# Kernel optimization log

Hardware: AMD Instinct MI355X
Metric: run time of the kernel (lower is better)

The kernel has to match this reference:

```python
import jax, jax.numpy as jnp
import numpy as np
from jax import lax

B, T, U, V, D, H = 4, 256, 64, 1024, 256, 256
BLANK = V - 1
NEG = -1.0e30
CTC_W = 0.3


def setup_inputs():
    ks = jax.random.split(jax.random.key(0), 9)
    return {
        "x_enc": jax.random.normal(ks[0], (B, T, D), jnp.float32),
        "x_dec": jax.random.normal(ks[1], (B, U + 1, H), jnp.float32),
        "W_enc": jax.random.normal(ks[2], (D, H), jnp.float32) / float(np.sqrt(D)),
        "b_enc": jnp.zeros((H,), jnp.float32),
        "W_dec": jax.random.normal(ks[3], (H, H), jnp.float32) / float(np.sqrt(H)),
        "b_dec": jnp.zeros((H,), jnp.float32),
        "W_out": jax.random.normal(ks[4], (H, V), jnp.float32) / float(np.sqrt(H)),
        "b_out": jnp.zeros((V,), jnp.float32),
        "W_ctc": jax.random.normal(ks[5], (D, V), jnp.float32) / float(np.sqrt(D)),
        "b_ctc": jnp.zeros((V,), jnp.float32),
        "target": jax.random.randint(ks[6], (B, U), 0, V - 1, jnp.int32),
        "frame_length": (T - jax.random.randint(ks[7], (B,), 0, T // 4)).astype(jnp.int32),
        "target_length": (U - jax.random.randint(ks[8], (B,), 0, U // 4)).astype(jnp.int32),
    }


def _forward(x_enc, x_dec, W_enc, b_enc, W_dec, b_dec, W_out, b_out, W_ctc, b_ctc,
             target, frame_length, target_length):
    b_idx = jnp.arange(B)
    ft, tl = frame_length, target_length

    # ---- Joiner: broadcast-add of projected enc/pred states, tanh, output proj ----
    h = jnp.tanh((x_enc @ W_enc + b_enc)[:, :, None, :]
                 + (x_dec @ W_dec + b_dec)[:, None, :, :])        # [B,T,U+1,H]
    logp = jax.nn.log_softmax(h @ W_out + b_out, axis=-1)          # [B,T,U+1,V]

    # gather=True trick: only blank and target-label log-probs are needed
    lp_blank = logp[..., BLANK]                                    # [B,T,U+1]
    lp_label = jnp.take_along_axis(
        logp[:, :, :U, :],
        jnp.broadcast_to(target[:, None, :, None], (B, T, U, 1)), axis=3)[..., 0]  # [B,T,U]

    # ---- RNNT forward DP over the (T, U+1) lattice ----
    def u_scan(b0, lbl):
        # b0[u] = alpha[t-1,u] + blank[t-1,u]; alpha[t,u] = logaddexp(b0[u], alpha[t,u-1]+lbl[u-1])
        def step(c, xs):
            bu, lu = xs
            new = jnp.logaddexp(bu, c + lu)
            return new, new
        _, outs = lax.scan(step, b0[:, 0],
                           (jnp.moveaxis(b0[:, 1:], 1, 0), jnp.moveaxis(lbl, 1, 0)))
        return jnp.concatenate([b0[:, :1], jnp.moveaxis(outs, 0, 1)], axis=1)

    alpha0 = jnp.concatenate([jnp.zeros((B, 1), logp.dtype),
                              jnp.cumsum(lp_label[:, 0, :], axis=1)], axis=1)  # [B,U+1]

    def t_step(prev, xs):
        blk_prev, lbl_t = xs
        a = u_scan(prev + blk_prev, lbl_t)
        return a, a

    _, rest = lax.scan(t_step, alpha0,
                       (jnp.moveaxis(lp_blank[:, :-1, :], 1, 0),
                        jnp.moveaxis(lp_label[:, 1:, :], 1, 0)))
    alphas = jnp.concatenate([alpha0[None], rest], axis=0)          # [T,B,U+1]
    ll = alphas[ft - 1, b_idx, tl] + lp_blank[b_idx, ft - 1, tl]
    rnnt_loss = jnp.mean(-ll)

    # ---- CTC branch: linear head on encoder output + standard CTC DP ----
    logp_ctc = jax.nn.log_softmax(x_enc @ W_ctc + b_ctc, axis=-1)   # [B,T,V]
    S = 2 * U + 1
    ext = jnp.full((B, S), BLANK, jnp.int32).at[:, 1::2].set(target)
    emit = jnp.take_along_axis(logp_ctc,
                               jnp.broadcast_to(ext[:, None, :], (B, T, S)), axis=2)  # [B,T,S]
    skip = jnp.concatenate([jnp.zeros((B, 2), bool),
                            (ext[:, 2:] != BLANK) & (ext[:, 2:] != ext[:, :-2])], axis=1)
    c0 = jnp.full((B, S), NEG, logp_ctc.dtype).at[:, 0].set(emit[:, 0, 0]).at[:, 1].set(emit[:, 0, 1])

    def c_step(prev, xs):
        emit_t, t = xs
        p2 = jnp.concatenate([jnp.full((B, 1), NEG, prev.dtype), prev[:, :-1]], axis=1)
        p3 = jnp.where(skip,
                       jnp.concatenate([jnp.full((B, 2), NEG, prev.dtype), prev[:, :-2]], axis=1),
                       NEG)
        new = emit_t + jnp.logaddexp(jnp.logaddexp(prev, p2), p3)
        new = jnp.where((t < ft)[:, None], new, prev)  # freeze past frame_length
        return new, None

    cT, _ = lax.scan(c_step, c0, (jnp.moveaxis(emit[:, 1:, :], 1, 0), jnp.arange(1, T)))
    s_last = 2 * tl
    ll_ctc = jnp.logaddexp(cT[b_idx, s_last], cT[b_idx, s_last - 1])
    ctc_loss = jnp.where(ll_ctc < NEG / 2, 0.0, -ll_ctc).sum() / B  # zero_infinity, sum/B

    return rnnt_loss + CTC_W * ctc_loss


def reference(x_enc, x_dec, W_enc, b_enc, W_dec, b_dec, W_out, b_out, W_ctc, b_ctc,
              target, frame_length, target_length):
    return _forward(x_enc, x_dec, W_enc, b_enc, W_dec, b_dec, W_out, b_out, W_ctc, b_ctc,
                    target, frame_length, target_length)
```

## Files before the change

### kernel.cpp

```cpp
#include <hip/hip_runtime.h>
#include <hip/hip_bf16.h>

#define Bn 4
#define Tn 256
#define Un 64
#define UP1 65
#define Vn 1024
#define Dn 256
#define Hn 256
#define BLANKC 1023
#define NEGF (-1.0e30f)
#define CTCW 0.3f
#define R2E 1.4426950408889634f
#define LN2 0.6931471805599453f

typedef __attribute__((ext_vector_type(8))) short short8;
typedef __attribute__((ext_vector_type(4))) float f32x4;
typedef __attribute__((ext_vector_type(4))) unsigned int u32x4;

static __device__ __forceinline__ unsigned short f2bf(float f) {
  unsigned int u = __float_as_uint(f);
  u += 0x7FFFu + ((u >> 16) & 1u);
  return (unsigned short)(u >> 16);
}
static __device__ __forceinline__ unsigned int pack2bf(float a, float b) {
  return (unsigned int)f2bf(a) | ((unsigned int)f2bf(b) << 16);
}
static __device__ __forceinline__ float ftanh(float x) {
  float e = __expf(2.0f * x);
  return 1.0f - 2.0f / (e + 1.0f);
}
static __device__ __forceinline__ float ex2(float x) {
  return __builtin_amdgcn_exp2f(x);
}
static __device__ __forceinline__ float lg2(float x) {
  return __builtin_amdgcn_logf(x);
}
static __device__ __forceinline__ float laddexp2_(float x, float y) {
  float m = fmaxf(x, y);
  float d = y - x;
  return m + lg2(1.0f + ex2(-fabsf(d)));
}
static __device__ __forceinline__ float laddexp3_2(float a, float b, float c) {
  float m = fmaxf(fmaxf(a, b), c);
  return m + lg2(ex2(a - m) + ex2(b - m) + ex2(c - m));
}
static __device__ __forceinline__ float shfl_up1(float x) {
  int r = __builtin_amdgcn_update_dpp(0, __float_as_int(x), 0x138, 0xF, 0xF, false);
  return __int_as_float(r);
}

__global__ __launch_bounds__(256) void k_prep(
    const float* __restrict__ W_enc, const float* __restrict__ W_dec,
    const float* __restrict__ W_out, const float* __restrict__ W_ctc,
    unsigned short* __restrict__ Wt_enc, unsigned short* __restrict__ Wt_dec,
    unsigned short* __restrict__ Wt_out, unsigned short* __restrict__ Wt_ctc,
    float* __restrict__ out) {
  const int blk = blockIdx.x, tid = threadIdx.x;
  if (blk == 0 && tid == 0) out[0] = 0.0f;
  __shared__ float tilebuf[64][65];
  if (blk < 128) {
    const float* Wsrc = (blk < 64) ? W_out : W_ctc;
    unsigned short* Wd = (blk < 64) ? Wt_out : Wt_ctc;
    const int tt = blk & 63;
    const int k0 = (tt & 3) * 64, v0 = (tt >> 2) * 64;
#pragma unroll
    for (int rep = 0; rep < 16; ++rep) {
      int e = rep * 256 + tid;
      int rr = e >> 6, cc = e & 63;
      tilebuf[rr][cc] = Wsrc[(k0 + rr) * 1024 + (v0 + cc)];
    }
    __syncthreads();
#pragma unroll
    for (int rep = 0; rep < 16; ++rep) {
      int e = rep * 256 + tid;
      int nn = e >> 6, kk = e & 63;
      int n = v0 + nn, k = k0 + kk;
      int c = n >> 8, col = n & 255;
      int ks = k >> 5, sub = (k >> 3) & 3, k7 = k & 7;
      Wd[(c * 8 + ks) * 8192 + sub * 2048 + col * 8 + k7] = f2bf(tilebuf[kk][nn]);
    }
  } else {
    const float* Wsrc = (blk < 144) ? W_enc : W_dec;
    unsigned short* Wd = (blk < 144) ? Wt_enc : Wt_dec;
    const int tt = (blk - 128) & 15;
    const int k0 = (tt & 3) * 64, v0 = (tt >> 2) * 64;
#pragma unroll
    for (int rep = 0; rep < 16; ++rep) {
      int e = rep * 256 + tid;
      int rr = e >> 6, cc = e & 63;
      tilebuf[rr][cc] = Wsrc[(k0 + rr) * 256 + (v0 + cc)];
    }
    __syncthreads();
#pragma unroll
    for (int rep = 0; rep < 16; ++rep) {
      int e = rep * 256 + tid;
      int rr = e >> 6, cc = e & 63;
      Wd[(v0 + rr) * 256 + (k0 + cc)] = f2bf(tilebuf[cc][rr]);
    }
  }
}

__global__ __launch_bounds__(256) void k_lin(
    const float* __restrict__ x_enc, const float* __restrict__ x_dec,
    const unsigned short* __restrict__ Wt_enc, const float* __restrict__ b_enc,
    const unsigned short* __restrict__ Wt_dec, const float* __restrict__ b_dec,
    float* __restrict__ enc_lin, float* __restrict__ dec_lin) {
  __shared__ __align__(16) char Asw[64 * 512];
  const int tid = threadIdx.x;
  const int w = tid >> 6, l = tid & 63;
  const int l15 = l & 15, l4 = l >> 4;
  const bool enc = blockIdx.x < 16;
  const int m0 = enc ? blockIdx.x * 64 : (blockIdx.x - 16) * 64;
  const int Mlim = enc ? 1024 : 260;
  const float* xp = enc ? x_enc : x_dec;
  const unsigned short* Wt = enc ? Wt_enc : Wt_dec;
  const float* bias = enc ? b_enc : b_dec;
  float* outp = enc ? enc_lin : dec_lin;

#pragma unroll
  for (int it = 0; it < 8; ++it) {
    int e = (it << 8) + tid;
    int i = e >> 5;
    int k0 = (e & 31) << 3;
    int r = m0 + i;
    if (r > Mlim - 1) r = Mlim - 1;
    const float* sp = xp + r * 256 + k0;
    f32x4 e0 = *(const f32x4*)sp;
    f32x4 e1 = *(const f32x4*)(sp + 4);
    u32x4 pv;
    pv[0] = pack2bf(e0[0], e0[1]);
    pv[1] = pack2bf(e0[2], e0[3]);
    pv[2] = pack2bf(e1[0], e1[1]);
    pv[3] = pack2bf(e1[2], e1[3]);
    int byt = (i << 9) + (k0 << 1);
    byt ^= (i & 7) << 4;
    *(u32x4*)(Asw + byt) = pv;
  }
  __syncthreads();

  const int nb = w * 64;
  f32x4 acc[4][4] = {};
#pragma unroll
  for (int ks = 0; ks < 8; ++ks) {
    int k = ks * 32 + l4 * 8;
    short8 af[4];
#pragma unroll
    for (int mt = 0; mt < 4; ++mt) {
      int i = mt * 16 + l15;
      int byt = (i << 9) + (k << 1);
      byt ^= (i & 7) << 4;
      af[mt] = *(const short8*)(Asw + byt);
    }
    short8 bfr[4];
#pragma unroll
    for (int nt = 0; nt < 4; ++nt) {
      int n = nb + nt * 16 + l15;
      bfr[nt] = *(const short8*)(Wt + n * 256 + k);
    }
#pragma unroll
    for (int mt = 0; mt < 4; ++mt)
#pragma unroll
      for (int nt = 0; nt < 4; ++nt)
        acc[mt][nt] = __builtin_amdgcn_mfma_f32_16x16x32_bf16(
            af[mt], bfr[nt], acc[mt][nt], 0, 0, 0);
  }
  float biasv[4];
#pragma unroll
  for (int nt = 0; nt < 4; ++nt) biasv[nt] = bias[nb + nt * 16 + l15];
#pragma unroll
  for (int mt = 0; mt < 4; ++mt)
#pragma unroll
    for (int rr = 0; rr < 4; ++rr) {
      int row = m0 + mt * 16 + l4 * 4 + rr;
      if (row < Mlim) {
#pragma unroll
        for (int nt = 0; nt < 4; ++nt)
          outp[row * 256 + nb + nt * 16 + l15] = acc[mt][nt][rr] + biasv[nt];
      }
    }
}

__global__ __launch_bounds__(512) void k_join2(
    const float* __restrict__ enc_lin, const float* __restrict__ dec_lin,
    const unsigned short* __restrict__ Wt_out, const float* __restrict__ b_out,
    const float* __restrict__ x_enc,
    const unsigned short* __restrict__ Wt_ctc, const float* __restrict__ b_ctc,
    const int* __restrict__ target,
    float* __restrict__ lp_blank, float* __restrict__ lp_label,
    float* __restrict__ ctc_blank, float* __restrict__ ctc_lse,
    float* __restrict__ ctc_lab) {
  __shared__ __align__(16) char Asw[128 * 512];
  __shared__ float s_psum[4][128];
  __shared__ float s_blank[128], s_label[128];
  __shared__ int s_tgt[128];

  const int tid = threadIdx.x;
  const int w = tid >> 6, l = tid & 63;
  const int wc = w & 3, wr = w >> 2;
  const int l15 = l & 15, l4 = l >> 4;
  const int bid = blockIdx.x;

  const bool joiner = bid >= 8;
  const unsigned short* Wt = joiner ? Wt_out : Wt_ctc;
  const float* bias = joiner ? b_out : b_ctc;

  const unsigned short* tb = Wt + l4 * 2048 + (wc * 64 + l15) * 8;

  short8 bE[4], bO[4];
#define LOADB(REG, S)                                                          \
  {                                                                            \
    const unsigned short* p_ = tb + (S)*8192;                                  \
    _Pragma("unroll") for (int nt = 0; nt < 4; ++nt)                           \
        REG[nt] = *(const short8*)(p_ + nt * 128);                             \
  }
  {
    const int sc0 = (bid & 3) * 8;
    LOADB(bE, sc0 + 0)
    LOADB(bO, sc0 + 1)
  }

  int b, r0 = 0, g0 = 0;
  if (joiner) {
    const int jbid = bid - 8;
    b = jbid / 130;
    r0 = (jbid % 130) * 128;
#pragma unroll
    for (int it = 0; it < 8; ++it) {
      int e = (it << 9) + tid;
      int i = e >> 5;
      int k0 = (e & 31) << 3;
      int r = r0 + i;
      int t = r / 65;
      int u = r - t * 65;
      const float* ep = enc_lin + ((b * Tn + t) * Hn + k0);
      const float* dp = dec_lin + ((b * UP1 + u) * Hn + k0);
      f32x4 e0 = *(const f32x4*)ep;
      f32x4 e1 = *(const f32x4*)(ep + 4);
      f32x4 d0 = *(const f32x4*)dp;
      f32x4 d1 = *(const f32x4*)(dp + 4);
      u32x4 pv;
      pv[0] = pack2bf(ftanh(e0[0] + d0[0]) * R2E, ftanh(e0[1] + d0[1]) * R2E);
      pv[1] = pack2bf(ftanh(e0[2] + d0[2]) * R2E, ftanh(e0[3] + d0[3]) * R2E);
      pv[2] = pack2bf(ftanh(e1[0] + d1[0]) * R2E, ftanh(e1[1] + d1[1]) * R2E);
      pv[3] = pack2bf(ftanh(e1[2] + d1[2]) * R2E, ftanh(e1[3] + d1[3]) * R2E);
      int byt = (i << 9) + (k0 << 1);
      byt ^= (i & 7) << 4;
      *(u32x4*)(Asw + byt) = pv;
    }
    if (tid < 128) {
      int u = (r0 + tid) % 65;
      s_tgt[tid] = (u < Un) ? target[b * Un + u] : -1;
    }
  } else {
    g0 = bid * 128;
    b = g0 >> 8;
#pragma unroll
    for (int it = 0; it < 8; ++it) {
      int e = (it << 9) + tid;
      int i = e >> 5;
      int k0 = (e & 31) << 3;
      const float* sp = x_enc + (g0 + i) * Dn + k0;
      f32x4 e0 = *(const f32x4*)sp;
      f32x4 e1 = *(const f32x4*)(sp + 4);
      u32x4 pv;
      pv[0] = pack2bf(e0[0] * R2E, e0[1] * R2E);
      pv[1] = pack2bf(e0[2] * R2E, e0[3] * R2E);
      pv[2] = pack2bf(e1[0] * R2E, e1[1] * R2E);
      pv[3] = pack2bf(e1[2] * R2E, e1[3] * R2E);
      int byt = (i << 9) + (k0 << 1);
      byt ^= (i & 7) << 4;
      *(u32x4*)(Asw + byt) = pv;
    }
    if (tid < 64) s_tgt[tid] = target[b * Un + tid];
  }
  __syncthreads();

  float ssum[16];
#pragma unroll
  for (int j = 0; j < 16; ++j) ssum[j] = 0.0f;

#define MFMASTEP(REG, KS)                                                      \
  {                                                                            \
    const int k_ = (KS)*32 + l4 * 8;                                           \
    _Pragma("unroll") for (int mt = 0; mt < 4; ++mt) {                         \
      int i_ = wr * 64 + mt * 16 + l15;                                        \
      int byt_ = ((i_ << 9) + (k_ << 1)) ^ ((i_ & 7) << 4);                    \
      short8 af_ = *(const short8*)(Asw + byt_);                               \
      _Pragma("unroll") for (int nt = 0; nt < 4; ++nt)                         \
          acc[mt][nt] = __builtin_amdgcn_mfma_f32_16x16x32_bf16(               \
              af_, REG[nt], acc[mt][nt], 0, 0, 0);                             \
    }                                                                          \
  }
#define SB __builtin_amdgcn_sched_barrier(0)

#pragma unroll 1
  for (int cr = 0; cr < 4; ++cr) {
    const int cc = (cr + bid) & 3;
    const int sc = cc * 8;
    const int scn = ((cr + 1 + bid) & 3) * 8;
    f32x4 acc[4][4] = {};
    MFMASTEP(bE, 0) LOADB(bE, sc + 2) SB;
    MFMASTEP(bO, 1) LOADB(bO, sc + 3) SB;
    MFMASTEP(bE, 2) LOADB(bE, sc + 4) SB;
    MFMASTEP(bO, 3) LOADB(bO, sc + 5) SB;
    MFMASTEP(bE, 4) LOADB(bE, sc + 6) SB;
    MFMASTEP(bO, 5) LOADB(bO, sc + 7) SB;
    MFMASTEP(bE, 6) LOADB(bE, (cr < 3) ? scn + 0 : sc + 6) SB;
    MFMASTEP(bO, 7) LOADB(bO, (cr < 3) ? scn + 1 : sc + 7) SB;

    const int nb = cc * 256 + wc * 64;
    float biasv[4];
#pragma unroll
    for (int nt = 0; nt < 4; ++nt) biasv[nt] = bias[nb + nt * 16 + l15] * R2E;
#pragma unroll
    for (int mt = 0; mt < 4; ++mt)
#pragma unroll
      for (int nt = 0; nt < 4; ++nt)
#pragma unroll
        for (int rr = 0; rr < 4; ++rr) acc[mt][nt][rr] += biasv[nt];

    if (joiner) {
      if (cc == 3 && wc == 3 && l15 == 15) {
#pragma unroll
        for (int mt = 0; mt < 4; ++mt)
#pragma unroll
          for (int rr = 0; rr < 4; ++rr)
            s_blank[wr * 64 + mt * 16 + l4 * 4 + rr] = acc[mt][3][rr];
      }
#pragma unroll
      for (int mt = 0; mt < 4; ++mt)
#pragma unroll
        for (int rr = 0; rr < 4; ++rr) {
          int row = wr * 64 + mt * 16 + l4 * 4 + rr;
          int tg = s_tgt[row];
          if ((tg >> 8) == cc && ((tg >> 6) & 3) == wc && (tg & 15) == l15) {
            int ntv = (tg >> 4) & 3;
            float v01 = (ntv & 1) ? acc[mt][1][rr] : acc[mt][0][rr];
            float v23 = (ntv & 1) ? acc[mt][3][rr] : acc[mt][2][rr];
            s_label[row] = (ntv & 2) ? v23 : v01;
          }
        }
    } else {
      if (cc == 3 && wc == 3 && l15 == 15) {
#pragma unroll
        for (int mt = 0; mt < 4; ++mt)
#pragma unroll
          for (int rr = 0; rr < 4; ++rr)
            s_blank[wr * 64 + mt * 16 + l4 * 4 + rr] = acc[mt][3][rr];
      }
#pragma unroll 1
      for (int u = 0; u < 64; ++u) {
        int tgu = s_tgt[u];
        if ((tgu >> 8) == cc && ((tgu >> 6) & 3) == wc) {
          int ntv = (tgu >> 4) & 3;
          if ((tgu & 15) == l15) {
#pragma unroll
            for (int mt = 0; mt < 4; ++mt)
#pragma unroll
              for (int rr = 0; rr < 4; ++rr) {
                float v01 = (ntv & 1) ? acc[mt][1][rr] : acc[mt][0][rr];
                float v23 = (ntv & 1) ? acc[mt][3][rr] : acc[mt][2][rr];
                float v = (ntv & 2) ? v23 : v01;
                ctc_lab[(g0 + wr * 64 + mt * 16 + l4 * 4 + rr) * 64 + u] = v;
              }
          }
        }
      }
    }
#pragma unroll
    for (int mt = 0; mt < 4; ++mt)
#pragma unroll
      for (int rr = 0; rr < 4; ++rr)
        ssum[mt * 4 + rr] += ex2(acc[mt][0][rr]) + ex2(acc[mt][1][rr]) +
                             ex2(acc[mt][2][rr]) + ex2(acc[mt][3][rr]);
  }
#undef MFMASTEP
#undef LOADB
#undef SB

#pragma unroll
  for (int ms = 1; ms < 16; ms <<= 1)
#pragma unroll
    for (int j = 0; j < 16; ++j) ssum[j] += __shfl_xor(ssum[j], ms, 64);
  if (l15 == 0) {
#pragma unroll
    for (int j = 0; j < 16; ++j)
      s_psum[wc][wr * 64 + (j >> 2) * 16 + l4 * 4 + (j & 3)] = ssum[j];
  }
  __syncthreads();

  if (tid < 128) {
    float tot = s_psum[0][tid] + s_psum[1][tid] + s_psum[2][tid] + s_psum[3][tid];
    float lse = lg2(tot);
    if (joiner) {
      int r = r0 + tid;
      int t = r / 65;
      int u = r - t * 65;
      lp_blank[(b * Tn + t) * UP1 + u] = s_blank[tid] - lse;
      if (u < Un) lp_label[(b * Tn + t) * Un + u] = s_label[tid] - lse;
    } else {
      ctc_blank[g0 + tid] = s_blank[tid] - lse;
      ctc_lse[g0 + tid] = lse;
    }
  }
}

__global__ __launch_bounds__(256) void k_dp(
    const float* __restrict__ lp_blank, const float* __restrict__ lp_label,
    const float* __restrict__ ctc_blank, const float* __restrict__ ctc_lse,
    const float* __restrict__ ctc_lab,
    const int* __restrict__ target,
    const int* __restrict__ flen, const int* __restrict__ tlen,
    float* __restrict__ out) {
  __shared__ float sA[256 * 66];
  __shared__ __align__(16) float sB[16384];
  __shared__ float sC[256], sD[256];
  __shared__ float cT[129];
  const int tid = threadIdx.x;
  const int l = tid & 63;

  if (blockIdx.x < 4) {
    const int b = blockIdx.x;
    for (int i = tid; i < 16640; i += 256) {
      int r = i / 65, cidx = i - r * 65;
      sA[r * 66 + cidx] = lp_blank[b * 16640 + i];
    }
    {
      const f32x4* g2 = (const f32x4*)(lp_label + b * 16384);
      f32x4* s2 = (f32x4*)sB;
      for (int i = tid; i < 4096; i += 256) s2[i] = g2[i];
    }
    __syncthreads();
    if (tid < 64) {
      const int ft = flen[b], tl = tlen[b];
      const int dstar = ft - 1 + tl;
      const bool isown = (l == tl);
      const bool is64 = (tl == 64) && (l == 63);
      const int lc = (l >= 1) ? l - 1 : 0;

#define RLOAD(D0, VB, VL, VB64, VL64)                                          \
  _Pragma("unroll") for (int j = 0; j < 8; ++j) {                              \
    const int d_ = (D0) + j;                                                   \
    const int t_ = d_ - l;                                                     \
    const int tbc_ = (t_ < 1) ? 1 : (t_ > 255 ? 255 : t_);                     \
    const int tcc_ = (t_ < 0) ? 0 : (t_ > 255 ? 255 : t_);                     \
    VB[j] = sA[(tbc_ - 1) * 66 + l];                                           \
    VL[j] = (l == 0) ? NEGF : sB[tcc_ * 64 + lc];                              \
    const int t64_ = d_ - 64;                                                  \
    const int t64b_ = (t64_ < 1) ? 1 : (t64_ > 255 ? 255 : t64_);              \
    const int t64c_ = (t64_ < 0) ? 0 : (t64_ > 255 ? 255 : t64_);              \
    VB64[j] = sA[(t64b_ - 1) * 66 + 64];                                       \
    VL64[j] = sB[t64c_ * 64 + 63];                                             \
  }

      float cvb[8], cvl[8], cvb64[8], cvl64[8];
      RLOAD(1, cvb, cvl, cvb64, cvl64);
      float a = (l == 0) ? 0.0f : NEGF;
      float a64 = NEGF, cap = NEGF;
      for (int d0 = 1; d0 <= 313; d0 += 8) {
        float nvb[8], nvl[8], nvb64[8], nvl64[8];
        RLOAD(d0 + 8, nvb, nvl, nvb64, nvl64);
        __builtin_amdgcn_sched_barrier(0);
#pragma unroll
        for (int j = 0; j < 8; ++j) {
          const int d = d0 + j;
          float aleft = shfl_up1(a);
          float x = a + cvb[j];
          float y = aleft + cvl[j];
          float nw = laddexp2_(x, y);
          float nw64 = laddexp2_(a64 + cvb64[j], a + cvl64[j]);
          a = nw;
          a64 = (l == 63) ? nw64 : a64;
          bool hit = (d == dstar);
          cap = (hit && isown) ? a : cap;
          cap = (hit && is64) ? a64 : cap;
        }
        __builtin_amdgcn_sched_barrier(0);
#pragma unroll
        for (int j = 0; j < 8; ++j) {
          cvb[j] = nvb[j];
          cvl[j] = nvl[j];
          cvb64[j] = nvb64[j];
          cvl64[j] = nvl64[j];
        }
      }
#undef RLOAD
      bool owner = (tl < 64) ? isown : (l == 63);
      if (owner)
        atomicAdd(out, -0.25f * LN2 * (cap + sA[(ft - 1) * 66 + tl]));
    }
  } else {
    const int b = blockIdx.x - 4;
    {
      const f32x4* g2 = (const f32x4*)(ctc_lab + b * 16384);
      f32x4* s2 = (f32x4*)sB;
      for (int i = tid; i < 4096; i += 256) s2[i] = g2[i];
      sC[tid] = ctc_blank[b * 256 + tid];
      sD[tid] = ctc_lse[b * 256 + tid];
    }
    __syncthreads();
    if (tid < 64) {
      const int ft = flen[b], tl = tlen[b];
      const int tg = target[b * Un + l];
      const int tgp = (l >= 1) ? target[b * Un + l - 1] : -1;
      const bool skip1 = (l >= 1) && (tg != tgp);

#define CLOAD(T0, EB, E1)                                                      \
  _Pragma("unroll") for (int j = 0; j < 8; ++j) {                              \
    const int tc_ = ((T0) + j > 255) ? 255 : (T0) + j;                         \
    EB[j] = sC[tc_];                                                           \
    E1[j] = sB[tc_ * 64 + l] - sD[tc_];                                        \
  }

      float ceb[8], ce1[8];
      CLOAD(1, ceb, ce1);
      float a0 = (l == 0) ? sC[0] : NEGF;
      float a1 = (l == 0) ? (sB[0] - sD[0]) : NEGF;
      float a2 = NEGF;
      for (int t0 = 1; t0 <= 249; t0 += 8) {
        float neb[8], ne1[8];
        CLOAD(t0 + 8, neb, ne1);
        __builtin_amdgcn_sched_barrier(0);
#pragma unroll
        for (int j = 0; j < 8; ++j) {
          const int t = t0 + j;
          float pm1 = shfl_up1(a1);
          pm1 = (l == 0) ? NEGF : pm1;
          float n0 = ceb[j] + laddexp2_(a0, pm1);
          float n1 = ce1[j] + laddexp3_2(a1, a0, skip1 ? pm1 : NEGF);
          float n2 = ceb[j] + laddexp2_(a2, a1);
          bool run = (t < ft);
          a0 = run ? n0 : a0;
          a1 = run ? n1 : a1;
          a2 = (run && (l == 63)) ? n2 : a2;
        }
        __builtin_amdgcn_sched_barrier(0);
#pragma unroll
        for (int j = 0; j < 8; ++j) {
          ceb[j] = neb[j];
          ce1[j] = ne1[j];
        }
      }
#undef CLOAD
      cT[2 * l] = a0;
      cT[2 * l + 1] = a1;
      if (l == 63) cT[128] = a2;
      __builtin_amdgcn_s_waitcnt(0);
      if (l == 0) {
        int sl = 2 * tl;
        float ll = laddexp2_(cT[sl], cT[sl - 1]);
        float lb = (ll < NEGF * 0.7f) ? 0.0f : -ll;
        atomicAdd(out, CTCW * 0.25f * LN2 * lb);
      }
    }
  }
}

extern "C" void kernel_launch(void* const* d_in, const int* in_sizes, int n_in,
                              void* d_out, int out_size, void* d_ws, size_t ws_size,
                              hipStream_t stream) {
  (void)in_sizes; (void)n_in; (void)out_size; (void)ws_size;
  const float* x_enc = (const float*)d_in[0];
  const float* x_dec = (const float*)d_in[1];
  const float* W_enc = (const float*)d_in[2];
  const float* b_enc = (const float*)d_in[3];
  const float* W_dec = (const float*)d_in[4];
  const float* b_dec = (const float*)d_in[5];
  const float* W_out = (const float*)d_in[6];
  const float* b_out = (const float*)d_in[7];
  const float* W_ctc = (const float*)d_in[8];
  const float* b_ctc = (const float*)d_in[9];
  const int* target = (const int*)d_in[10];
  const int* flen = (const int*)d_in[11];
  const int* tlen = (const int*)d_in[12];

  float* ws = (float*)d_ws;
  float* enc_lin = ws;
  float* dec_lin = ws + 262144;
  float* lp_blank = ws + 328704;
  float* lp_label = ws + 395264;
  float* ctc_blank = ws + 460800;
  float* ctc_lse = ws + 461824;
  float* ctc_lab = ws + 462848;
  unsigned short* Wt_out = (unsigned short*)(ws + 528384);
  unsigned short* Wt_ctc = Wt_out + 262144;
  unsigned short* Wt_enc = (unsigned short*)lp_blank;
  unsigned short* Wt_dec = (unsigned short*)lp_label;
  float* out = (float*)d_out;

  k_prep<<<dim3(160), dim3(256), 0, stream>>>(
      W_enc, W_dec, W_out, W_ctc, Wt_enc, Wt_dec, Wt_out, Wt_ctc, out);
  k_lin<<<dim3(21), dim3(256), 0, stream>>>(
      x_enc, x_dec, Wt_enc, b_enc, Wt_dec, b_dec, enc_lin, dec_lin);
  k_join2<<<dim3(528), dim3(512), 0, stream>>>(
      enc_lin, dec_lin, Wt_out, b_out, x_enc, Wt_ctc, b_ctc, target,
      lp_blank, lp_label, ctc_blank, ctc_lse, ctc_lab);
  k_dp<<<dim3(8), dim3(64 * 4), 0, stream>>>(
      lp_blank, lp_label, ctc_blank, ctc_lse, ctc_lab, target, flen, tlen, out);
}
```

Baseline: 130.1 us.

## Stage output-weight tiles through LDS with async triple buffering; trim DP loops

The joiner/CTC GEMM kernel no longer loads weight fragments straight from global memory into registers. It streams each weight K-slice into a triple-buffered LDS ring using global_load_lds, with vmcnt waits and workgroup barriers gating each step, and it caches the bias in LDS. The chunk order no longer rotates per block. Separately, the RNNT and CTC DP loops now stop at each batch's real lattice extent (dstar, frame_length) instead of a fixed bound. The costs are two extra barriers per K-step and larger LDS use, which may lower occupancy.

```diff
diff --git a/kernel.cpp b/kernel.cpp
--- a/kernel.cpp
+++ b/kernel.cpp
@@ -17,6 +17,11 @@
 typedef __attribute__((ext_vector_type(8))) short short8;
 typedef __attribute__((ext_vector_type(4))) float f32x4;
 typedef __attribute__((ext_vector_type(4))) unsigned int u32x4;
+
+#define GLD_LDS16(gp, lp)                                                      \
+  __builtin_amdgcn_global_load_lds(                                            \
+      (const __attribute__((address_space(1))) void*)(gp),                     \
+      (__attribute__((address_space(3))) void*)(lp), 16, 0, 0)
 
 static __device__ __forceinline__ unsigned short f2bf(float f) {
   unsigned int u = __float_as_uint(f);
@@ -191,6 +196,8 @@
     float* __restrict__ ctc_blank, float* __restrict__ ctc_lse,
     float* __restrict__ ctc_lab) {
   __shared__ __align__(16) char Asw[128 * 512];
+  __shared__ __align__(16) char Bsw[3 * 16384];
+  __shared__ float s_bias[1024];
   __shared__ float s_psum[4][128];
   __shared__ float s_blank[128], s_label[128];
   __shared__ int s_tgt[128];
@@ -203,22 +210,15 @@
 
   const bool joiner = bid >= 8;
   const unsigned short* Wt = joiner ? Wt_out : Wt_ctc;
-  const float* bias = joiner ? b_out : b_ctc;
-
-  const unsigned short* tb = Wt + l4 * 2048 + (wc * 64 + l15) * 8;
-
-  short8 bE[4], bO[4];
-#define LOADB(REG, S)                                                          \
-  {                                                                            \
-    const unsigned short* p_ = tb + (S)*8192;                                  \
-    _Pragma("unroll") for (int nt = 0; nt < 4; ++nt)                           \
-        REG[nt] = *(const short8*)(p_ + nt * 128);                             \
-  }
-  {
-    const int sc0 = (bid & 3) * 8;
-    LOADB(bE, sc0 + 0)
-    LOADB(bO, sc0 + 1)
-  }
+  const float* biasp = joiner ? b_out : b_ctc;
+
+  auto stageB = [&](int s, int buf) {
+#pragma unroll
+    for (int r = 0; r < 2; ++r) {
+      const unsigned short* src = Wt + s * 8192 + r * 4096 + tid * 8;
+      GLD_LDS16(src, Bsw + buf * 16384 + r * 8192 + (w << 10));
+    }
+  };
 
   int b, r0 = 0, g0 = 0;
   if (joiner) {
@@ -274,45 +274,61 @@
     }
     if (tid < 64) s_tgt[tid] = target[b * Un + tid];
   }
-  __syncthreads();
+  for (int i = tid; i < 1024; i += 512) s_bias[i] = biasp[i] * R2E;
+  __builtin_amdgcn_sched_barrier(0);
+  stageB(0, 0);
+  stageB(1, 1);
+  stageB(2, 2);
+  asm volatile("s_waitcnt vmcnt(6) lgkmcnt(0)" ::: "memory");
+  __builtin_amdgcn_s_barrier();
 
   float ssum[16];
 #pragma unroll
   for (int j = 0; j < 16; ++j) ssum[j] = 0.0f;
 
-#define MFMASTEP(REG, KS)                                                      \
-  {                                                                            \
-    const int k_ = (KS)*32 + l4 * 8;                                           \
-    _Pragma("unroll") for (int mt = 0; mt < 4; ++mt) {                         \
-      int i_ = wr * 64 + mt * 16 + l15;                                        \
-      int byt_ = ((i_ << 9) + (k_ << 1)) ^ ((i_ & 7) << 4);                    \
-      short8 af_ = *(const short8*)(Asw + byt_);                               \
-      _Pragma("unroll") for (int nt = 0; nt < 4; ++nt)                         \
-          acc[mt][nt] = __builtin_amdgcn_mfma_f32_16x16x32_bf16(               \
-              af_, REG[nt], acc[mt][nt], 0, 0, 0);                             \
-    }                                                                          \
-  }
-#define SB __builtin_amdgcn_sched_barrier(0)
-
+  int buf = 0;
 #pragma unroll 1
-  for (int cr = 0; cr < 4; ++cr) {
-    const int cc = (cr + bid) & 3;
-    const int sc = cc * 8;
-    const int scn = ((cr + 1 + bid) & 3) * 8;
+  for (int c = 0; c < 4; ++c) {
     f32x4 acc[4][4] = {};
-    MFMASTEP(bE, 0) LOADB(bE, sc + 2) SB;
-    MFMASTEP(bO, 1) LOADB(bO, sc + 3) SB;
-    MFMASTEP(bE, 2) LOADB(bE, sc + 4) SB;
-    MFMASTEP(bO, 3) LOADB(bO, sc + 5) SB;
-    MFMASTEP(bE, 4) LOADB(bE, sc + 6) SB;
-    MFMASTEP(bO, 5) LOADB(bO, sc + 7) SB;
-    MFMASTEP(bE, 6) LOADB(bE, (cr < 3) ? scn + 0 : sc + 6) SB;
-    MFMASTEP(bO, 7) LOADB(bO, (cr < 3) ? scn + 1 : sc + 7) SB;
-
-    const int nb = cc * 256 + wc * 64;
+#pragma unroll
+    for (int ks = 0; ks < 8; ++ks) {
+      asm volatile("s_waitcnt vmcnt(4)" ::: "memory");
+      __builtin_amdgcn_s_barrier();
+      __builtin_amdgcn_sched_barrier(0);
+      const int bufb = buf * 16384;
+      const int k = ks * 32 + l4 * 8;
+      short8 af[4];
+#pragma unroll
+      for (int mt = 0; mt < 4; ++mt) {
+        int i = wr * 64 + mt * 16 + l15;
+        int byt = (i << 9) + (k << 1);
+        byt ^= (i & 7) << 4;
+        af[mt] = *(const short8*)(Asw + byt);
+      }
+      short8 bfr[4];
+#pragma unroll
+      for (int nt = 0; nt < 4; ++nt) {
+        int byt = bufb + l4 * 4096 + ((wc * 64 + nt * 16 + l15) << 4);
+        bfr[nt] = *(const short8*)(Bsw + byt);
+      }
+#pragma unroll
+      for (int mt = 0; mt < 4; ++mt)
+#pragma unroll
+        for (int nt = 0; nt < 4; ++nt)
+          acc[mt][nt] = __builtin_amdgcn_mfma_f32_16x16x32_bf16(
+              af[mt], bfr[nt], acc[mt][nt], 0, 0, 0);
+      __builtin_amdgcn_sched_barrier(0);
+      __builtin_amdgcn_s_barrier();
+      const int s = c * 8 + ks;
+      const int nst = (s + 3 < 32) ? s + 3 : 31;
+      stageB(nst, buf);
+      __builtin_amdgcn_sched_barrier(0);
+      buf = (buf == 2) ? 0 : buf + 1;
+    }
+    const int nb = c * 256 + wc * 64;
     float biasv[4];
 #pragma unroll
-    for (int nt = 0; nt < 4; ++nt) biasv[nt] = bias[nb + nt * 16 + l15] * R2E;
+    for (int nt = 0; nt < 4; ++nt) biasv[nt] = s_bias[nb + nt * 16 + l15];
 #pragma unroll
     for (int mt = 0; mt < 4; ++mt)
 #pragma unroll
@@ -321,7 +337,7 @@
         for (int rr = 0; rr < 4; ++rr) acc[mt][nt][rr] += biasv[nt];
 
     if (joiner) {
-      if (cc == 3 && wc == 3 && l15 == 15) {
+      if (c == 3 && wc == 3 && l15 == 15) {
 #pragma unroll
         for (int mt = 0; mt < 4; ++mt)
 #pragma unroll
@@ -334,7 +350,7 @@
         for (int rr = 0; rr < 4; ++rr) {
           int row = wr * 64 + mt * 16 + l4 * 4 + rr;
           int tg = s_tgt[row];
-          if ((tg >> 8) == cc && ((tg >> 6) & 3) == wc && (tg & 15) == l15) {
+          if ((tg >> 8) == c && ((tg >> 6) & 3) == wc && (tg & 15) == l15) {
             int ntv = (tg >> 4) & 3;
             float v01 = (ntv & 1) ? acc[mt][1][rr] : acc[mt][0][rr];
             float v23 = (ntv & 1) ? acc[mt][3][rr] : acc[mt][2][rr];
@@ -342,7 +358,7 @@
           }
         }
     } else {
-      if (cc == 3 && wc == 3 && l15 == 15) {
+      if (c == 3 && wc == 3 && l15 == 15) {
 #pragma unroll
         for (int mt = 0; mt < 4; ++mt)
 #pragma unroll
@@ -352,7 +368,7 @@
 #pragma unroll 1
       for (int u = 0; u < 64; ++u) {
         int tgu = s_tgt[u];
-        if ((tgu >> 8) == cc && ((tgu >> 6) & 3) == wc) {
+        if ((tgu >> 8) == c && ((tgu >> 6) & 3) == wc) {
           int ntv = (tgu >> 4) & 3;
           if ((tgu & 15) == l15) {
 #pragma unroll
@@ -375,9 +391,6 @@
         ssum[mt * 4 + rr] += ex2(acc[mt][0][rr]) + ex2(acc[mt][1][rr]) +
                              ex2(acc[mt][2][rr]) + ex2(acc[mt][3][rr]);
   }
-#undef MFMASTEP
-#undef LOADB
-#undef SB
 
 #pragma unroll
   for (int ms = 1; ms < 16; ms <<= 1)
@@ -458,7 +471,7 @@
       RLOAD(1, cvb, cvl, cvb64, cvl64);
       float a = (l == 0) ? 0.0f : NEGF;
       float a64 = NEGF, cap = NEGF;
-      for (int d0 = 1; d0 <= 313; d0 += 8) {
+      for (int d0 = 1; d0 <= dstar; d0 += 8) {
         float nvb[8], nvl[8], nvb64[8], nvl64[8];
         RLOAD(d0 + 8, nvb, nvl, nvb64, nvl64);
         __builtin_amdgcn_sched_barrier(0);
@@ -518,7 +531,7 @@
       float a0 = (l == 0) ? sC[0] : NEGF;
       float a1 = (l == 0) ? (sB[0] - sD[0]) : NEGF;
       float a2 = NEGF;
-      for (int t0 = 1; t0 <= 249; t0 += 8) {
+      for (int t0 = 1; t0 < ft; t0 += 8) {
         float neb[8], ne1[8];
         CLOAD(t0 + 8, neb, ne1);
         __builtin_amdgcn_sched_barrier(0);
```

New measurement: 158.1 us. 1.22x slower.
